# Kernel optimization log

Hardware: AMD Instinct MI355X
Metric: run time of the kernel (lower is better)

Reference implementation:

```python
import jax, jax.numpy as jnp
import numpy as np

N_NODES = 100000
N_EDGES = 6400000
N_IN, E_HID, E_OUT = 768, 512, 256
HID, HEADS, N_CLASSES = 32, 2, 3
NEG_SLOPE = 0.2


def setup_inputs() -> dict:
    key = jax.random.key(0)
    ks = jax.random.split(key, 12)
    def glorot(k, shape):
        fan_in, fan_out = shape[0], shape[-1]
        lim = (6.0 / (fan_in + fan_out)) ** 0.5
        return jax.random.uniform(k, shape, jnp.float32, -lim, lim)
    return {
        "x": jax.random.normal(ks[0], (N_NODES, N_IN), jnp.float32),
        "edge_index": jax.random.randint(ks[1], (2, N_EDGES), 0, N_NODES, jnp.int64),
        "W_e1": glorot(ks[2], (N_IN, E_HID)),
        "b_e1": jnp.zeros((E_HID,), jnp.float32),
        "W_e2": glorot(ks[3], (E_HID, E_OUT)),
        "b_e2": jnp.zeros((E_OUT,), jnp.float32),
        "W_lin": glorot(ks[4], (E_OUT, HID)),
        "b_lin": jnp.zeros((HID,), jnp.float32),
        "W_att": glorot(ks[5], (HID, HEADS * N_CLASSES)),  # GATConv lin (no bias)
        "att_src": glorot(ks[6], (HEADS, N_CLASSES)),
        "att_dst": glorot(ks[7], (HEADS, N_CLASSES)),
        "bias": jnp.zeros((N_CLASSES,), jnp.float32),
    }


def reference(x, edge_index, W_e1, b_e1, W_e2, b_e2, W_lin, b_lin,
              W_att, att_src, att_dst, bias):
    # embedder (Linear-ReLU-Linear) then linear projection to hid
    h = jax.nn.relu(x @ W_e1 + b_e1)
    h = h @ W_e2 + b_e2
    h = h @ W_lin + b_lin                     # [N, hid]
    # GATConv(hid -> n_classes, heads=2, concat=False), add_self_loops=True
    N = h.shape[0]
    hh = (h @ W_att).reshape(N, HEADS, N_CLASSES)      # [N, H, C]
    a_src = jnp.sum(hh * att_src, axis=-1)             # [N, H]
    a_dst = jnp.sum(hh * att_dst, axis=-1)             # [N, H]
    loop = jnp.arange(N, dtype=edge_index.dtype)
    src = jnp.concatenate([edge_index[0], loop])       # [E+N]
    dst = jnp.concatenate([edge_index[1], loop])
    alpha = jax.nn.leaky_relu(a_src[src] + a_dst[dst], NEG_SLOPE)  # [E+N, H]
    # segment softmax over destination node (every segment nonempty via self-loops)
    amax = jax.ops.segment_max(alpha, dst, num_segments=N)
    alpha = jnp.exp(alpha - amax[dst])
    denom = jax.ops.segment_sum(alpha, dst, num_segments=N)
    alpha = alpha / denom[dst]                         # [E+N, H]
    msg = alpha[:, :, None] * hh[src]                  # [E+N, H, C]
    out = jax.ops.segment_sum(msg, dst, num_segments=N)  # [N, H, C]
    return out.mean(axis=1) + bias                     # concat=False -> mean over heads
```

## Files before the change

kernel.cpp:

```cpp
#include <hip/hip_runtime.h>


#define NNODES 100000
#define NEDGES 6400000
#define DIN    768
#define DH1    512
#define DH2    256
#define NEG_SLOPE 0.2f
#define SCAN_NB 391
#define LDSP   40

typedef __bf16 bf16x8 __attribute__((ext_vector_type(8)));
typedef float  f32x4  __attribute__((ext_vector_type(4)));

__device__ __forceinline__ float bf2f(unsigned short h) {
    return __uint_as_float(((unsigned)h) << 16);
}
__device__ __forceinline__ unsigned short f2bf(float f) {
    unsigned u = __float_as_uint(f);
    unsigned r = u + 0x7FFFu + ((u >> 16) & 1u);
    return (unsigned short)(r >> 16);
}
__device__ __forceinline__ float ldf(const void* p, int i, int isf32) {
    return isf32 ? ((const float*)p)[i] : bf2f(((const unsigned short*)p)[i]);
}
__device__ __forceinline__ uint4 packbf8(const float* p) {
    float4 u = *(const float4*)p;
    float4 v = *(const float4*)(p + 4);
    uint4 r;
    r.x = (unsigned)f2bf(u.x) | ((unsigned)f2bf(u.y) << 16);
    r.y = (unsigned)f2bf(u.z) | ((unsigned)f2bf(u.w) << 16);
    r.z = (unsigned)f2bf(v.x) | ((unsigned)f2bf(v.y) << 16);
    r.w = (unsigned)f2bf(v.z) | ((unsigned)f2bf(v.w) << 16);
    return r;
}

__global__ void detect_dtypes(const unsigned short* x, const unsigned short* we1,
                              const unsigned short* we2, const unsigned short* wlin,
                              const unsigned short* watt, const int* ei, int* flags) {
    __shared__ int cnt;
    int b = blockIdx.x, t = threadIdx.x;
    if (t == 0) cnt = 0;
    __syncthreads();
    if (b < 5) {
        const unsigned short* p = (b == 0) ? x : (b == 1) ? we1 : (b == 2) ? we2
                                  : (b == 3) ? wlin : watt;
        int K = (b == 4) ? 96 : 512;
        int c = 0;
        for (int i = t; i < K; i += 256) {
            int e = (p[2 * i] >> 7) & 0xFF;
            if (e >= 0x66 && e <= 0x8C) c++;
        }
        atomicAdd(&cnt, c);
        __syncthreads();
        if (t == 0) flags[b] = (cnt * 10 < K * 6) ? 1 : 0;
    } else {
        int c = 0;
        for (int i = t; i < 2048; i += 256)
            if (ei[2 * i + 1] != 0) c++;
        atomicAdd(&cnt, c);
        __syncthreads();
        if (t == 0) { flags[5] = (cnt == 0) ? 1 : 0; flags[15] = 0; }
    }
}

__global__ void transpose_conv(const void* in, unsigned short* out, int K, int N,
                               const int* flags, int fidx) {
    int f32 = flags[fidx];
    int idx = blockIdx.x * 256 + threadIdx.x;
    if (idx >= K * N) return;
    int k = idx / N, n = idx - k * N;
    unsigned short v = f32 ? f2bf(((const float*)in)[idx])
                           : ((const unsigned short*)in)[idx];
    out[(size_t)n * K + k] = v;
}

template <bool RELU>
__global__ __launch_bounds__(256)
void gemm_bt(const void* __restrict__ A,
             const unsigned short* __restrict__ Bt,
             const unsigned short* __restrict__ bias,
             unsigned short* __restrict__ C,
             int M, int K, int N, const int* flags, int aidx, int nt_n) {
    __shared__ unsigned short sA[128 * LDSP];
    __shared__ unsigned short sB[128 * LDSP];
    const int af32 = flags[aidx];
    const int tid = threadIdx.x;

    const int nwg = gridDim.x;
    const int bid = blockIdx.x;
    const int xcd = bid & 7, bidx = bid >> 3;
    const int q = nwg >> 3, r = nwg & 7;
    const int logical = (xcd < r ? xcd * (q + 1) : r * (q + 1) + (xcd - r) * q) + bidx;
    const int m0 = (logical / nt_n) * 128;
    const int n0 = (logical % nt_n) * 128;

    const int srow = tid >> 2;
    const int scol = (tid & 3) * 8;
    int ar0 = m0 + srow;      if (ar0 >= M) ar0 = M - 1;
    int ar1 = m0 + 64 + srow; if (ar1 >= M) ar1 = M - 1;
    const unsigned short* Ah = (const unsigned short*)A;
    const float*          Af = (const float*)A;
    const unsigned short* gA0h = Ah + (size_t)ar0 * K + scol;
    const unsigned short* gA1h = Ah + (size_t)ar1 * K + scol;
    const float*          gA0f = Af + (size_t)ar0 * K + scol;
    const float*          gA1f = Af + (size_t)ar1 * K + scol;
    const unsigned short* gB0 = Bt + (size_t)(n0 + srow) * K + scol;
    const unsigned short* gB1 = Bt + (size_t)(n0 + 64 + srow) * K + scol;

    const int wave = tid >> 6, lane = tid & 63;
    const int wr = wave >> 1, wc = wave & 1;
    const int lr = lane & 15;
    const int lk = (lane >> 4) * 8;
    f32x4 acc[4][4] = {};

    for (int k0 = 0; k0 < K; k0 += 32) {
        uint4 a0, a1;
        if (af32) { a0 = packbf8(gA0f + k0); a1 = packbf8(gA1f + k0); }
        else      { a0 = *(const uint4*)(gA0h + k0); a1 = *(const uint4*)(gA1h + k0); }
        uint4 b0 = *(const uint4*)(gB0 + k0);
        uint4 b1 = *(const uint4*)(gB1 + k0);
        __syncthreads();
        *(uint4*)&sA[srow * LDSP + scol]        = a0;
        *(uint4*)&sA[(64 + srow) * LDSP + scol] = a1;
        *(uint4*)&sB[srow * LDSP + scol]        = b0;
        *(uint4*)&sB[(64 + srow) * LDSP + scol] = b1;
        __syncthreads();
        bf16x8 aF[4], bF[4];
#pragma unroll
        for (int i = 0; i < 4; i++) aF[i] = *(const bf16x8*)&sA[(wr * 64 + i * 16 + lr) * LDSP + lk];
#pragma unroll
        for (int j = 0; j < 4; j++) bF[j] = *(const bf16x8*)&sB[(wc * 64 + j * 16 + lr) * LDSP + lk];
#pragma unroll
        for (int i = 0; i < 4; i++)
#pragma unroll
            for (int j = 0; j < 4; j++)
                acc[i][j] = __builtin_amdgcn_mfma_f32_16x16x32_bf16(aF[i], bF[j], acc[i][j], 0, 0, 0);
    }

    float bv[4];
#pragma unroll
    for (int j = 0; j < 4; j++) bv[j] = bf2f(bias[n0 + wc * 64 + j * 16 + lr]);
#pragma unroll
    for (int i = 0; i < 4; i++) {
        int rbase = m0 + wr * 64 + i * 16 + (lane >> 4) * 4;
#pragma unroll
        for (int r = 0; r < 4; r++) {
            int row = rbase + r;
            if (row < M) {
                size_t base = (size_t)row * N + n0 + wc * 64 + lr;
#pragma unroll
                for (int j = 0; j < 4; j++) {
                    float v = acc[i][j][r] + bv[j];
                    if (RELU) v = fmaxf(v, 0.f);
                    C[base + j * 16] = f2bf(v);
                }
            }
        }
    }
}

__global__ __launch_bounds__(256)
void node_att(const unsigned short* __restrict__ h2,
              const void* __restrict__ Wlin,
              const unsigned short* __restrict__ blin,
              const void* __restrict__ Watt,
              const void* __restrict__ attS,
              const void* __restrict__ attD,
              float* __restrict__ hh, float* __restrict__ asrc,
              float* __restrict__ adst, const int* flags) {
    __shared__ float sW[256 * 32];
    __shared__ float sh2[8 * 256];
    __shared__ float sH[8 * 32];
    __shared__ float sHH[8 * 6];
    const int wlf = flags[3], waf = flags[4];
    const int tid = threadIdx.x;
    for (int i = tid; i < 256 * 32; i += 256) sW[i] = ldf(Wlin, i, wlf);
    const int n0 = blockIdx.x * 8;
    {
        int e = tid * 8;
        int r = e >> 8;
        int c = e & 255;
        uint4 v = *(const uint4*)(h2 + (size_t)(n0 + r) * 256 + c);
        float* o = &sh2[r * 256 + c];
        o[0] = __uint_as_float(v.x << 16); o[1] = __uint_as_float(v.x & 0xFFFF0000u);
        o[2] = __uint_as_float(v.y << 16); o[3] = __uint_as_float(v.y & 0xFFFF0000u);
        o[4] = __uint_as_float(v.z << 16); o[5] = __uint_as_float(v.z & 0xFFFF0000u);
        o[6] = __uint_as_float(v.w << 16); o[7] = __uint_as_float(v.w & 0xFFFF0000u);
    }
    __syncthreads();
    const int nl = tid >> 5;
    const int c  = tid & 31;
    float acc = bf2f(blin[c]);
    const float* hrow = &sh2[nl * 256];
#pragma unroll 8
    for (int k = 0; k < 256; k++) acc += hrow[k] * sW[k * 32 + c];
    sH[nl * 32 + c] = acc;
    __syncthreads();
    if (tid < 48) {
        int n = tid / 6, j = tid - (tid / 6) * 6;
        float s = 0.f;
#pragma unroll
        for (int k = 0; k < 32; k++) s += sH[n * 32 + k] * ldf(Watt, k * 6 + j, waf);
        sHH[n * 6 + j] = s;
        hh[(size_t)(n0 + n) * 6 + j] = s;
    }
    __syncthreads();
    if (tid < 16) {
        int n = tid >> 1, hd = tid & 1;
        float s = 0.f, d = 0.f;
#pragma unroll
        for (int cc = 0; cc < 3; cc++) {
            float v = sHH[n * 6 + hd * 3 + cc];
            s += v * ldf(attS, hd * 3 + cc, waf);
            d += v * ldf(attD, hd * 3 + cc, waf);
        }
        asrc[(size_t)(n0 + n) * 2 + hd] = s;
        adst[(size_t)(n0 + n) * 2 + hd] = d;
    }
}

__global__ void init_zero(int* __restrict__ p, int n) {
    int i = blockIdx.x * 256 + threadIdx.x;
    if (i < n) p[i] = 0;
}

__global__ __launch_bounds__(256)
void edge_rank(const int* __restrict__ ei, int* __restrict__ count,
               int* __restrict__ rank, const int* __restrict__ flags) {
    int e = blockIdx.x * 256 + threadIdx.x;
    if (e >= NEDGES) return;
    int d;
    if (flags[5]) d = (int)((const long long*)ei)[NEDGES + e];
    else          d = ei[NEDGES + e];
    rank[e] = atomicAdd(&count[d], 1);
}

__global__ void scan_block_sums(const int* __restrict__ count, int* __restrict__ bsum) {
    __shared__ int s[256];
    int i = blockIdx.x * 256 + threadIdx.x;
    int t = threadIdx.x;
    s[t] = (i < NNODES) ? count[i] : 0;
    __syncthreads();
    for (int off = 128; off > 0; off >>= 1) {
        if (t < off) s[t] += s[t + off];
        __syncthreads();
    }
    if (t == 0) bsum[blockIdx.x] = s[0];
}

__global__ void scan_bsum(const int* __restrict__ bsum, int* __restrict__ bscan, int nb) {
    __shared__ int s[512];
    int t = threadIdx.x;
    int v = (t < nb) ? bsum[t] : 0;
    s[t] = v;
    __syncthreads();
    for (int off = 1; off < 512; off <<= 1) {
        int x = (t >= off) ? s[t - off] : 0;
        __syncthreads();
        s[t] += x;
        __syncthreads();
    }
    if (t < nb) bscan[t] = s[t] - v;
}

__global__ void scan_final(const int* __restrict__ count, const int* __restrict__ bscan,
                           int* __restrict__ offs) {
    __shared__ int s[256];
    int i = blockIdx.x * 256 + threadIdx.x;
    int t = threadIdx.x;
    int v = (i < NNODES) ? count[i] : 0;
    s[t] = v;
    __syncthreads();
    for (int off = 1; off < 256; off <<= 1) {
        int x = (t >= off) ? s[t - off] : 0;
        __syncthreads();
        s[t] += x;
        __syncthreads();
    }
    if (i < NNODES) offs[i] = s[t] - v + bscan[blockIdx.x];
}

__global__ __launch_bounds__(256)
void edge_scatter(const int* __restrict__ ei, const int* __restrict__ rank,
                  const int* __restrict__ offs, int* __restrict__ sorted,
                  const int* __restrict__ flags) {
    int e = blockIdx.x * 256 + threadIdx.x;
    if (e >= NEDGES) return;
    int s, d;
    if (flags[5]) {
        const long long* e64 = (const long long*)ei;
        s = (int)e64[e];
        d = (int)e64[NEDGES + e];
    } else {
        s = ei[e];
        d = ei[NEDGES + e];
    }
    sorted[offs[d] + rank[e]] = s;
}

__global__ __launch_bounds__(256)
void gather_finalize(const int* __restrict__ sorted, const int* __restrict__ offs,
                     const int* __restrict__ count,
                     const float* __restrict__ asrc, const float* __restrict__ adst,
                     const float* __restrict__ hh,
                     const unsigned short* __restrict__ bias,
                     void* __restrict__ out, const int* __restrict__ flags) {
    int w = blockIdx.x * 4 + (threadIdx.x >> 6);
    if (w >= NNODES) return;
    int lane = threadIdx.x & 63;
    int base = offs[w];
    int cnt  = count[w];
    float2 ad = *(const float2*)(adst + 2 * (size_t)w);

    float d0 = 0.f, d1 = 0.f;
    float n0 = 0.f, n1 = 0.f, n2 = 0.f, n3 = 0.f, n4 = 0.f, n5 = 0.f;
    for (int k = lane; k < cnt; k += 64) {
        int s = sorted[base + k];
        float2 as = *(const float2*)(asrc + 2 * (size_t)s);
        float a0 = as.x + ad.x; a0 = a0 > 0.f ? a0 : NEG_SLOPE * a0;
        float a1 = as.y + ad.y; a1 = a1 > 0.f ? a1 : NEG_SLOPE * a1;
        float p0 = __expf(fminf(a0, 60.f));
        float p1 = __expf(fminf(a1, 60.f));
        const float* hs = hh + 6 * (size_t)s;
        d0 += p0; d1 += p1;
        n0 += p0 * hs[0]; n1 += p0 * hs[1]; n2 += p0 * hs[2];
        n3 += p1 * hs[3]; n4 += p1 * hs[4]; n5 += p1 * hs[5];
    }
#pragma unroll
    for (int m = 32; m > 0; m >>= 1) {
        d0 += __shfl_xor(d0, m, 64); d1 += __shfl_xor(d1, m, 64);
        n0 += __shfl_xor(n0, m, 64); n1 += __shfl_xor(n1, m, 64);
        n2 += __shfl_xor(n2, m, 64); n3 += __shfl_xor(n3, m, 64);
        n4 += __shfl_xor(n4, m, 64); n5 += __shfl_xor(n5, m, 64);
    }
    if (lane == 0) {
        float2 as = *(const float2*)(asrc + 2 * (size_t)w);
        float a0 = as.x + ad.x; a0 = a0 > 0.f ? a0 : NEG_SLOPE * a0;
        float a1 = as.y + ad.y; a1 = a1 > 0.f ? a1 : NEG_SLOPE * a1;
        float p0 = __expf(fminf(a0, 60.f));
        float p1 = __expf(fminf(a1, 60.f));
        const float* hw = hh + 6 * (size_t)w;
        d0 += p0; d1 += p1;
        n0 += p0 * hw[0]; n1 += p0 * hw[1]; n2 += p0 * hw[2];
        n3 += p1 * hw[3]; n4 += p1 * hw[4]; n5 += p1 * hw[5];

        float o0 = 0.5f * (n0 / d0 + n3 / d1) + bf2f(bias[0]);
        float o1 = 0.5f * (n1 / d0 + n4 / d1) + bf2f(bias[1]);
        float o2 = 0.5f * (n2 / d0 + n5 / d1) + bf2f(bias[2]);
        if (flags[0]) {
            float* o = (float*)out;
            o[3 * (size_t)w + 0] = o0; o[3 * (size_t)w + 1] = o1; o[3 * (size_t)w + 2] = o2;
        } else {
            unsigned short* o = (unsigned short*)out;
            o[3 * (size_t)w + 0] = f2bf(o0); o[3 * (size_t)w + 1] = f2bf(o1); o[3 * (size_t)w + 2] = f2bf(o2);
        }
    }
}

extern "C" void kernel_launch(void* const* d_in, const int* in_sizes, int n_in,
                              void* d_out, int out_size, void* d_ws, size_t ws_size,
                              hipStream_t stream) {
    const unsigned short* x    = (const unsigned short*)d_in[0];
    const int*            ei   = (const int*)d_in[1];
    const unsigned short* We1  = (const unsigned short*)d_in[2];
    const unsigned short* be1  = (const unsigned short*)d_in[3];
    const unsigned short* We2  = (const unsigned short*)d_in[4];
    const unsigned short* be2  = (const unsigned short*)d_in[5];
    const unsigned short* Wlin = (const unsigned short*)d_in[6];
    const unsigned short* blin = (const unsigned short*)d_in[7];
    const unsigned short* Watt = (const unsigned short*)d_in[8];
    const unsigned short* attS = (const unsigned short*)d_in[9];
    const unsigned short* attD = (const unsigned short*)d_in[10];
    const unsigned short* bias = (const unsigned short*)d_in[11];

    char* ws = (char*)d_ws;
    unsigned short* W1t   = (unsigned short*)(ws + 0);
    unsigned short* W2t   = (unsigned short*)(ws + 786432);
    unsigned short* h2    = (unsigned short*)(ws + 1048576);
    float*    hh    = (float*)(ws + 52248576);
    float*    asrc  = (float*)(ws + 54648576);
    float*    adst  = (float*)(ws + 55448576);
    int*      count = (int*)(ws + 56248576);
    int*      offs  = (int*)(ws + 56648576);
    int*      bsum  = (int*)(ws + 57048576);
    int*      bscan = (int*)(ws + 57052672);
    int*      flags = (int*)(ws + 59448576);
    unsigned short* h1 = (unsigned short*)(ws + 59448640);
    int* rank   = (int*)(ws + 59448640);
    int* sorted = (int*)(ws + 59448640 + 25600000);
    (void)ws_size; (void)in_sizes; (void)n_in; (void)out_size;

    detect_dtypes<<<6, 256, 0, stream>>>(x, We1, We2, Wlin, Watt, ei, flags);

    transpose_conv<<<(DIN * DH1 + 255) / 256, 256, 0, stream>>>(We1, W1t, DIN, DH1, flags, 1);
    transpose_conv<<<(DH1 * DH2 + 255) / 256, 256, 0, stream>>>(We2, W2t, DH1, DH2, flags, 2);

    dim3 blk(256);
    int nwg1 = ((NNODES + 127) / 128) * (DH1 / 128);
    gemm_bt<true><<<nwg1, blk, 0, stream>>>(x, W1t, be1, h1, NNODES, DIN, DH1,
                                            flags, 0, DH1 / 128);
    int nwg2 = ((NNODES + 127) / 128) * (DH2 / 128);
    gemm_bt<false><<<nwg2, blk, 0, stream>>>(h1, W2t, be2, h2, NNODES, DH1, DH2,
                                             flags, 15, DH2 / 128);

    node_att<<<NNODES / 8, 256, 0, stream>>>(h2, Wlin, blin, Watt, attS, attD,
                                             hh, asrc, adst, flags);

    init_zero<<<(NNODES + 255) / 256, 256, 0, stream>>>(count, NNODES);
    edge_rank<<<NEDGES / 256, 256, 0, stream>>>(ei, count, rank, flags);
    scan_block_sums<<<SCAN_NB, 256, 0, stream>>>(count, bsum);
    scan_bsum<<<1, 512, 0, stream>>>(bsum, bscan, SCAN_NB);
    scan_final<<<SCAN_NB, 256, 0, stream>>>(count, bscan, offs);
    edge_scatter<<<NEDGES / 256, 256, 0, stream>>>(ei, rank, offs, sorted, flags);
    gather_finalize<<<(NNODES + 3) / 4, 256, 0, stream>>>(sorted, offs, count,
                                                          asrc, adst, hh, bias,
                                                          d_out, flags);
}
```

Before: 1.281 ms.

## Replace global-atomic counting sort with two-pass bucketed CSR build

Edges are bucketed by destination high bits (256 nodes per bucket) using per-chunk LDS histograms, a per-bucket scan, and a scatter of (src,dst) pairs into bucket regions. Each bucket is then locally counted, scanned and scattered in LDS to produce count, offs and the sorted source array. This replaces 6.4M global atomics on a 100K-entry count array and the fully random scatter with LDS atomics and more localized writes. The cost is an extra pass over an 8-byte pair buffer and larger workspace use. Edge order within a node may differ from before, so floating-point summation order can change.

```diff
diff --git a/kernel.cpp b/kernel.cpp
--- a/kernel.cpp
+++ b/kernel.cpp
@@ -7,8 +7,10 @@
 #define DH1    512
 #define DH2    256
 #define NEG_SLOPE 0.2f
-#define SCAN_NB 391
 #define LDSP   40
+#define CHUNK  8192
+#define NPART  782
+#define NBUK   391
 
 typedef __bf16 bf16x8 __attribute__((ext_vector_type(8)));
 typedef float  f32x4  __attribute__((ext_vector_type(4)));
@@ -220,83 +222,134 @@
     }
 }
 
-__global__ void init_zero(int* __restrict__ p, int n) {
-    int i = blockIdx.x * 256 + threadIdx.x;
-    if (i < n) p[i] = 0;
-}
-
-__global__ __launch_bounds__(256)
-void edge_rank(const int* __restrict__ ei, int* __restrict__ count,
-               int* __restrict__ rank, const int* __restrict__ flags) {
-    int e = blockIdx.x * 256 + threadIdx.x;
-    if (e >= NEDGES) return;
-    int d;
-    if (flags[5]) d = (int)((const long long*)ei)[NEDGES + e];
-    else          d = ei[NEDGES + e];
-    rank[e] = atomicAdd(&count[d], 1);
-}
-
-__global__ void scan_block_sums(const int* __restrict__ count, int* __restrict__ bsum) {
-    __shared__ int s[256];
-    int i = blockIdx.x * 256 + threadIdx.x;
+
+__global__ __launch_bounds__(256)
+void part_hist(const int* __restrict__ ei, unsigned* __restrict__ histG,
+               const int* __restrict__ flags) {
+    __shared__ unsigned h[NBUK];
+    int k = blockIdx.x, t = threadIdx.x;
+    for (int i = t; i < NBUK; i += 256) h[i] = 0;
+    __syncthreads();
+    int e0 = k * CHUNK;
+    int e1 = e0 + CHUNK; if (e1 > NEDGES) e1 = NEDGES;
+    int i64 = flags[5];
+    for (int e = e0 + t; e < e1; e += 256) {
+        int d = i64 ? (int)((const long long*)ei)[NEDGES + e] : ei[NEDGES + e];
+        atomicAdd(&h[d >> 8], 1u);
+    }
+    __syncthreads();
+    for (int i = t; i < NBUK; i += 256) histG[(size_t)i * NPART + k] = h[i];
+}
+
+__global__ __launch_bounds__(256)
+void part_scan(const unsigned* __restrict__ histG, unsigned* __restrict__ start,
+               unsigned* __restrict__ btot) {
+    int b = blockIdx.x, t = threadIdx.x;
+    const unsigned* col = histG + (size_t)b * NPART;
+    unsigned* out = start + (size_t)b * NPART;
+    unsigned v[4]; unsigned sum = 0;
+#pragma unroll
+    for (int i = 0; i < 4; i++) {
+        int k = t * 4 + i;
+        unsigned x = (k < NPART) ? col[k] : 0;
+        v[i] = x; sum += x;
+    }
+    __shared__ unsigned s[256];
+    s[t] = sum; __syncthreads();
+    for (int off = 1; off < 256; off <<= 1) {
+        unsigned x = (t >= off) ? s[t - off] : 0;
+        __syncthreads();
+        s[t] += x;
+        __syncthreads();
+    }
+    unsigned ex = s[t] - sum;
+    unsigned run = ex;
+#pragma unroll
+    for (int i = 0; i < 4; i++) {
+        int k = t * 4 + i;
+        if (k < NPART) out[k] = run;
+        run += v[i];
+    }
+    if (t == 255) btot[b] = s[255];
+}
+
+__global__ void bucket_base(const unsigned* __restrict__ btot, unsigned* __restrict__ bbase) {
+    __shared__ unsigned s[512];
     int t = threadIdx.x;
-    s[t] = (i < NNODES) ? count[i] : 0;
-    __syncthreads();
-    for (int off = 128; off > 0; off >>= 1) {
-        if (t < off) s[t] += s[t + off];
-        __syncthreads();
-    }
-    if (t == 0) bsum[blockIdx.x] = s[0];
-}
-
-__global__ void scan_bsum(const int* __restrict__ bsum, int* __restrict__ bscan, int nb) {
-    __shared__ int s[512];
-    int t = threadIdx.x;
-    int v = (t < nb) ? bsum[t] : 0;
+    unsigned v = (t < NBUK) ? btot[t] : 0;
     s[t] = v;
     __syncthreads();
     for (int off = 1; off < 512; off <<= 1) {
-        int x = (t >= off) ? s[t - off] : 0;
+        unsigned x = (t >= off) ? s[t - off] : 0;
         __syncthreads();
         s[t] += x;
         __syncthreads();
     }
-    if (t < nb) bscan[t] = s[t] - v;
-}
-
-__global__ void scan_final(const int* __restrict__ count, const int* __restrict__ bscan,
-                           int* __restrict__ offs) {
-    __shared__ int s[256];
-    int i = blockIdx.x * 256 + threadIdx.x;
-    int t = threadIdx.x;
-    int v = (i < NNODES) ? count[i] : 0;
-    s[t] = v;
-    __syncthreads();
+    if (t < NBUK) bbase[t] = s[t] - v;
+    if (t == NBUK - 1) bbase[NBUK] = s[t];
+}
+
+__global__ __launch_bounds__(256)
+void part_scatter(const int* __restrict__ ei, const unsigned* __restrict__ start,
+                  const unsigned* __restrict__ bbase, uint2* __restrict__ pairs,
+                  const int* __restrict__ flags) {
+    __shared__ unsigned cur[NBUK];
+    int k = blockIdx.x, t = threadIdx.x;
+    for (int i = t; i < NBUK; i += 256)
+        cur[i] = bbase[i] + start[(size_t)i * NPART + k];
+    __syncthreads();
+    int e0 = k * CHUNK;
+    int e1 = e0 + CHUNK; if (e1 > NEDGES) e1 = NEDGES;
+    int i64 = flags[5];
+    for (int e = e0 + t; e < e1; e += 256) {
+        int s, d;
+        if (i64) {
+            const long long* E = (const long long*)ei;
+            s = (int)E[e];
+            d = (int)E[NEDGES + e];
+        } else {
+            s = ei[e];
+            d = ei[NEDGES + e];
+        }
+        unsigned pos = atomicAdd(&cur[d >> 8], 1u);
+        pairs[pos] = make_uint2((unsigned)s, (unsigned)d);
+    }
+}
+
+__global__ __launch_bounds__(256)
+void bucket_csr(const uint2* __restrict__ pairs, const unsigned* __restrict__ bbase,
+                int* __restrict__ count, int* __restrict__ offs,
+                int* __restrict__ sorted) {
+    int b = blockIdx.x, t = threadIdx.x;
+    unsigned e0 = bbase[b], e1 = bbase[b + 1];
+    int d0n = b << 8;
+    int nd = NNODES - d0n; if (nd > 256) nd = 256;
+    __shared__ unsigned cnt[256], s[256], cur[256];
+    cnt[t] = 0;
+    __syncthreads();
+    for (unsigned e = e0 + t; e < e1; e += 256)
+        atomicAdd(&cnt[pairs[e].y & 255], 1u);
+    __syncthreads();
+    unsigned myc = cnt[t];
+    s[t] = myc; __syncthreads();
     for (int off = 1; off < 256; off <<= 1) {
-        int x = (t >= off) ? s[t - off] : 0;
+        unsigned x = (t >= off) ? s[t - off] : 0;
         __syncthreads();
         s[t] += x;
         __syncthreads();
     }
-    if (i < NNODES) offs[i] = s[t] - v + bscan[blockIdx.x];
-}
-
-__global__ __launch_bounds__(256)
-void edge_scatter(const int* __restrict__ ei, const int* __restrict__ rank,
-                  const int* __restrict__ offs, int* __restrict__ sorted,
-                  const int* __restrict__ flags) {
-    int e = blockIdx.x * 256 + threadIdx.x;
-    if (e >= NEDGES) return;
-    int s, d;
-    if (flags[5]) {
-        const long long* e64 = (const long long*)ei;
-        s = (int)e64[e];
-        d = (int)e64[NEDGES + e];
-    } else {
-        s = ei[e];
-        d = ei[NEDGES + e];
-    }
-    sorted[offs[d] + rank[e]] = s;
+    unsigned ex = s[t] - myc;
+    if (t < nd) {
+        count[d0n + t] = (int)myc;
+        offs[d0n + t]  = (int)(e0 + ex);
+    }
+    cur[t] = e0 + ex;
+    __syncthreads();
+    for (unsigned e = e0 + t; e < e1; e += 256) {
+        uint2 p = pairs[e];
+        unsigned pos = atomicAdd(&cur[p.y & 255], 1u);
+        sorted[pos] = (int)p.x;
+    }
 }
 
 __global__ __launch_bounds__(256)
@@ -383,12 +436,14 @@
     float*    adst  = (float*)(ws + 55448576);
     int*      count = (int*)(ws + 56248576);
     int*      offs  = (int*)(ws + 56648576);
-    int*      bsum  = (int*)(ws + 57048576);
-    int*      bscan = (int*)(ws + 57052672);
+    unsigned* btot  = (unsigned*)(ws + 57048576);
+    unsigned* bbase = (unsigned*)(ws + 57052672);
     int*      flags = (int*)(ws + 59448576);
     unsigned short* h1 = (unsigned short*)(ws + 59448640);
-    int* rank   = (int*)(ws + 59448640);
-    int* sorted = (int*)(ws + 59448640 + 25600000);
+    uint2*    pairs  = (uint2*)(ws + 59448640);
+    int*      sorted = (int*)(ws + 110648640);
+    unsigned* histG  = (unsigned*)(ws + 136248640);
+    unsigned* start  = (unsigned*)(ws + 137471744);
     (void)ws_size; (void)in_sizes; (void)n_in; (void)out_size;
 
     detect_dtypes<<<6, 256, 0, stream>>>(x, We1, We2, Wlin, Watt, ei, flags);
@@ -407,12 +462,11 @@
     node_att<<<NNODES / 8, 256, 0, stream>>>(h2, Wlin, blin, Watt, attS, attD,
                                              hh, asrc, adst, flags);
 
-    init_zero<<<(NNODES + 255) / 256, 256, 0, stream>>>(count, NNODES);
-    edge_rank<<<NEDGES / 256, 256, 0, stream>>>(ei, count, rank, flags);
-    scan_block_sums<<<SCAN_NB, 256, 0, stream>>>(count, bsum);
-    scan_bsum<<<1, 512, 0, stream>>>(bsum, bscan, SCAN_NB);
-    scan_final<<<SCAN_NB, 256, 0, stream>>>(count, bscan, offs);
-    edge_scatter<<<NEDGES / 256, 256, 0, stream>>>(ei, rank, offs, sorted, flags);
+    part_hist<<<NPART, 256, 0, stream>>>(ei, histG, flags);
+    part_scan<<<NBUK, 256, 0, stream>>>(histG, start, btot);
+    bucket_base<<<1, 512, 0, stream>>>(btot, bbase);
+    part_scatter<<<NPART, 256, 0, stream>>>(ei, start, bbase, pairs, flags);
+    bucket_csr<<<NBUK, 256, 0, stream>>>(pairs, bbase, count, offs, sorted);
     gather_finalize<<<(NNODES + 3) / 4, 256, 0, stream>>>(sorted, offs, count,
                                                           asrc, adst, hh, bias,
                                                           d_out, flags);
```

Measured after the change: 1.061 ms. 17.2% less time.
